# Performance work log

Hardware: AMD Instinct MI355X
Metric: run time of the kernel (lower is better)

The kernel has to match this reference:

```python
import jax, jax.numpy as jnp
import numpy as np

N_NODES = 200000
N_EDGES = 400000
N_GRAPHS = 4096
IN_DIM, HID_DIM, OUT_DIM, EDGE_DIM = 128, 256, 256, 16


def setup_inputs() -> dict:
    key = jax.random.key(0)
    ks = jax.random.split(key, 16)
    x = jax.random.normal(ks[0], (N_NODES, IN_DIM), dtype=jnp.float32)
    edge_attr = jax.random.normal(ks[1], (N_EDGES, EDGE_DIM), dtype=jnp.float32)
    edge_index = jax.random.randint(ks[2], (2, N_EDGES), 0, N_NODES, dtype=jnp.int64)
    batch = jnp.sort(jax.random.randint(ks[3], (N_NODES,), 0, N_GRAPHS, dtype=jnp.int64))

    def lin(k, fan_in, fan_out):
        bound = 1.0 / np.sqrt(fan_in)
        kw, kb = jax.random.split(k)
        W = jax.random.uniform(kw, (fan_in, fan_out), minval=-bound, maxval=bound, dtype=jnp.float32)
        b = jax.random.uniform(kb, (fan_out,), minval=-bound, maxval=bound, dtype=jnp.float32)
        return W, b

    We1, be1 = lin(ks[4], EDGE_DIM, IN_DIM)    # GINEConv1 edge projection
    W1a, b1a = lin(ks[5], IN_DIM, HID_DIM)     # conv1 MLP layer 1
    W1b, b1b = lin(ks[6], HID_DIM, HID_DIM)    # conv1 MLP layer 2
    We2, be2 = lin(ks[7], EDGE_DIM, HID_DIM)   # GINEConv2 edge projection
    W2a, b2a = lin(ks[8], HID_DIM, HID_DIM)    # conv2 MLP layer 1
    W2b, b2b = lin(ks[9], HID_DIM, OUT_DIM)    # conv2 MLP layer 2
    return {"x": x, "edge_attr": edge_attr,
            "We1": We1, "be1": be1, "W1a": W1a, "b1a": b1a, "W1b": W1b, "b1b": b1b,
            "We2": We2, "be2": be2, "W2a": W2a, "b2a": b2a, "W2b": W2b, "b2b": b2b,
            "edge_index": edge_index, "batch": batch}


def _gine_conv(x, edge_attr, src, dst, We, be, Wa, ba, Wb, bb):
    # messages: relu(x_j + lin_edge(e)), scatter-add into destination nodes
    e_proj = edge_attr @ We + be                      # [E, D]
    msg = jax.nn.relu(x[src] + e_proj)                # [E, D]
    aggr = jax.ops.segment_sum(msg, dst, num_segments=x.shape[0])  # [N, D]
    h = x + aggr                                      # (1 + eps) * x_i + aggr, eps=0
    h = jax.nn.relu(h @ Wa + ba)
    return h @ Wb + bb


def reference(x, edge_attr, We1, be1, W1a, b1a, W1b, b1b,
              We2, be2, W2a, b2a, W2b, b2b, edge_index, batch):
    src, dst = edge_index[0], edge_index[1]
    h = jax.nn.relu(_gine_conv(x, edge_attr, src, dst, We1, be1, W1a, b1a, W1b, b1b))
    h = jax.nn.relu(_gine_conv(h, edge_attr, src, dst, We2, be2, W2a, b2a, W2b, b2b))
    # global mean pool over graphs
    sums = jax.ops.segment_sum(h, batch, num_segments=N_GRAPHS)            # [G, D]
    counts = jax.ops.segment_sum(jnp.ones((h.shape[0],), h.dtype), batch,
                                 num_segments=N_GRAPHS)                    # [G]
    return sums / jnp.maximum(counts, 1.0)[:, None]
```

## Files before the change

kernel.cpp:

```cpp
#include <hip/hip_runtime.h>
#include <hip/hip_bf16.h>

typedef float f32x4 __attribute__((ext_vector_type(4)));
typedef float f32x2 __attribute__((ext_vector_type(2)));
typedef unsigned short u16x2 __attribute__((ext_vector_type(2)));
typedef unsigned short u16x4 __attribute__((ext_vector_type(4)));
typedef unsigned short u16x8 __attribute__((ext_vector_type(8)));
typedef short s16x8 __attribute__((ext_vector_type(8)));

#define NN 200000
#define NE 400000
#define NG 4096
#define SCHUNK 1024
#define NSCAN ((NN + SCHUNK - 1) / SCHUNK)

template<int C> struct VecT;
template<> struct VecT<2> { using T = u16x2; };
template<> struct VecT<4> { using T = u16x4; };

__device__ __forceinline__ unsigned short f2bf(float f) {
    union { float f; unsigned int u; } v; v.f = f;
    unsigned int r = v.u + 0x7FFF + ((v.u >> 16) & 1);
    return (unsigned short)(r >> 16);
}
__device__ __forceinline__ float bf2f(unsigned short b) {
    union { unsigned int u; float f; } v; v.u = ((unsigned int)b) << 16;
    return v.f;
}

__global__ void detect_i64(const int* __restrict__ ei, int* __restrict__ flag) {
    unsigned long long m = __ballot(ei[threadIdx.x * 2 + 1] == 0);
    if (threadIdx.x == 0) *flag = (~m == 0ULL) ? 1 : 0;
}
__device__ __forceinline__ int load_idx(const int* p, long long i, int f64) {
    return f64 ? (int)((const long long*)p)[i] : p[i];
}

__global__ __launch_bounds__(256) void bat_conv(const int* __restrict__ bat,
                                                const int* __restrict__ flag,
                                                int* __restrict__ bat32) {
    int i = blockIdx.x * 256 + threadIdx.x;
    if (i < NN) bat32[i] = *flag ? (int)((const long long*)bat)[i] : bat[i];
}

__global__ void wt_conv(const float* __restrict__ W, unsigned short* __restrict__ Wt,
                        int K, int N) {
    int tid = blockIdx.x * 256 + threadIdx.x;
    if (tid >= K * N) return;
    int n = tid / K, k = tid - n * K;
    Wt[tid] = f2bf(W[(size_t)k * N + n]);
}

__global__ __launch_bounds__(256) void x2bf(const float* __restrict__ x,
                                            unsigned short* __restrict__ xh) {
    long long i = ((long long)blockIdx.x * 256 + threadIdx.x) * 4;
    if (i >= (long long)NN * 128) return;
    f32x4 v = *(const f32x4*)(x + i);
    u16x4 o; o.x = f2bf(v.x); o.y = f2bf(v.y); o.z = f2bf(v.z); o.w = f2bf(v.w);
    *(u16x4*)(xh + i) = o;
}

__global__ __launch_bounds__(256) void ea_perm(const float* __restrict__ ea,
                                               const int* __restrict__ eidx,
                                               const int* __restrict__ totE_p,
                                               float* __restrict__ eac) {
    int j = blockIdx.x * 256 + threadIdx.x;
    if (j >= *totE_p) return;
    int e = eidx[j];
    if ((unsigned)e >= NE) e = 0;
    const float* s = ea + (size_t)e * 16;
    float* d = eac + (size_t)j * 16;
#pragma unroll
    for (int k = 0; k < 4; ++k)
        *(f32x4*)(d + k * 4) = *(const f32x4*)(s + k * 4);
}

__global__ __launch_bounds__(256) void hist_dst(const int* __restrict__ ei,
                                                const int* __restrict__ flag,
                                                int* __restrict__ deg) {
    int e = blockIdx.x * 256 + threadIdx.x;
    if (e >= NE) return;
    int f64 = *flag;
    int s = load_idx(ei, e, f64);
    int d = load_idx(ei, (long long)NE + e, f64);
    if ((unsigned)s < NN && (unsigned)d < NN) atomicAdd(&deg[d], 1);
}

__global__ __launch_bounds__(256) void scan_bsum(const int* __restrict__ deg,
                                                 int* __restrict__ bsum) {
    __shared__ int red[256];
    int t = threadIdx.x, base = blockIdx.x * SCHUNK + t * 4;
    int s = 0;
#pragma unroll
    for (int c = 0; c < 4; ++c) { int i = base + c; if (i < NN) s += deg[i]; }
    red[t] = s; __syncthreads();
    for (int o = 128; o > 0; o >>= 1) { if (t < o) red[t] += red[t + o]; __syncthreads(); }
    if (t == 0) bsum[blockIdx.x] = red[0];
}

__global__ void scan_carry(int* __restrict__ bsum, int* __restrict__ rowptr_end) {
    if (threadIdx.x == 0) {
        int run = 0;
        for (int i = 0; i < NSCAN; ++i) { int v = bsum[i]; bsum[i] = run; run += v; }
        *rowptr_end = run;
    }
}

__global__ __launch_bounds__(256) void scan_final(const int* __restrict__ deg,
                                                  const int* __restrict__ bsum,
                                                  int* __restrict__ rowptr,
                                                  int* __restrict__ cursor) {
    __shared__ int lds[256];
    int t = threadIdx.x, base = blockIdx.x * SCHUNK + t * 4;
    int v[4], s = 0;
#pragma unroll
    for (int c = 0; c < 4; ++c) { int i = base + c; v[c] = (i < NN) ? deg[i] : 0; s += v[c]; }
    lds[t] = s; __syncthreads();
    for (int o = 1; o < 256; o <<= 1) {
        int x = 0;
        if (t >= o) x = lds[t - o];
        __syncthreads();
        if (t >= o) lds[t] += x;
        __syncthreads();
    }
    int run = lds[t] - s + bsum[blockIdx.x];
#pragma unroll
    for (int c = 0; c < 4; ++c) {
        int i = base + c;
        if (i < NN) { rowptr[i] = run; cursor[i] = run; }
        run += v[c];
    }
}

__global__ __launch_bounds__(256) void fill_csr(const int* __restrict__ ei,
                                                const int* __restrict__ flag,
                                                int* __restrict__ cursor,
                                                int* __restrict__ srcs,
                                                int* __restrict__ eidx) {
    int e = blockIdx.x * 256 + threadIdx.x;
    if (e >= NE) return;
    int f64 = *flag;
    int s = load_idx(ei, e, f64);
    int d = load_idx(ei, (long long)NE + e, f64);
    if ((unsigned)s >= NN || (unsigned)d >= NN) return;
    int pos = atomicAdd(&cursor[d], 1);
    if ((unsigned)pos < NE) { srcs[pos] = s; eidx[pos] = e; }
}

template<int C, int U>
__global__ __launch_bounds__(256)
void msg_build(const unsigned short* __restrict__ xh,
               const float* __restrict__ eac,
               const float* __restrict__ We, const float* __restrict__ be,
               const int* __restrict__ srcs, const int* __restrict__ totE_p,
               unsigned short* __restrict__ M) {
    using XV = typename VecT<C>::T;
    constexpr int D = 64 * C;
    constexpr int C2 = C / 2;
    const int wid  = (blockIdx.x * 256 + threadIdx.x) >> 6;
    const int lane = threadIdx.x & 63;
    const int totE = *totE_p;
    const int col = lane * C;

    f32x2 w2[16][C2], bb2[C2];
#pragma unroll
    for (int k = 0; k < 16; ++k)
#pragma unroll
        for (int c = 0; c < C2; ++c)
            w2[k][c] = *(const f32x2*)(We + k * D + col + 2 * c);
#pragma unroll
    for (int c = 0; c < C2; ++c) bb2[c] = *(const f32x2*)(be + col + 2 * c);

    const int j0 = wid * U;
    int sv[U];
    XV xv[U];
#pragma unroll
    for (int u = 0; u < U; ++u) {
        int j = j0 + u;
        sv[u] = (j < totE) ? srcs[j] : -1;
    }
#pragma unroll
    for (int u = 0; u < U; ++u) {
        if ((unsigned)sv[u] < NN)
            xv[u] = *(const XV*)(xh + (size_t)sv[u] * D + col);
        else
            xv[u] = (XV)0;
    }
#pragma unroll
    for (int u = 0; u < U; ++u) {
        int j = j0 + u;
        if (j >= totE) continue;
        const float* eap = eac + (size_t)j * 16;
        f32x4 e0 = *(const f32x4*)eap;
        f32x4 e1 = *(const f32x4*)(eap + 4);
        f32x4 e2 = *(const f32x4*)(eap + 8);
        f32x4 e3 = *(const f32x4*)(eap + 12);
        f32x2 m2[C2];
#pragma unroll
        for (int c = 0; c < C2; ++c) {
            f32x2 xx; xx.x = bf2f(xv[u][2 * c]); xx.y = bf2f(xv[u][2 * c + 1]);
            m2[c] = bb2[c] + xx;
        }
#pragma unroll
        for (int k = 0; k < 4; ++k) {
            f32x2 k0; k0.x = e0[k]; k0.y = e0[k];
            f32x2 k1; k1.x = e1[k]; k1.y = e1[k];
            f32x2 k2; k2.x = e2[k]; k2.y = e2[k];
            f32x2 k3; k3.x = e3[k]; k3.y = e3[k];
#pragma unroll
            for (int c = 0; c < C2; ++c) {
                m2[c] += k0 * w2[k][c];
                m2[c] += k1 * w2[4 + k][c];
                m2[c] += k2 * w2[8 + k][c];
                m2[c] += k3 * w2[12 + k][c];
            }
        }
        XV o;
#pragma unroll
        for (int c = 0; c < C2; ++c) {
            o[2 * c]     = f2bf(fmaxf(m2[c].x, 0.f));
            o[2 * c + 1] = f2bf(fmaxf(m2[c].y, 0.f));
        }
        *(XV*)(M + (size_t)j * D + col) = o;
    }
}

template<int C>
__global__ __launch_bounds__(256)
void seg_sum(const unsigned short* __restrict__ M, const int* __restrict__ rowptr,
             const unsigned short* __restrict__ self, unsigned short* __restrict__ outp) {
    using XV = typename VecT<C>::T;
    constexpr int D = 64 * C;
    const int node = (blockIdx.x * 256 + threadIdx.x) >> 6;
    const int lane = threadIdx.x & 63;
    if (node >= NN) return;
    const int col = lane * C;
    int lo = rowptr[node], hi = rowptr[node + 1];
    if (lo > hi || (unsigned)hi > NE) { lo = 0; hi = 0; }

    float a[C];
    XV sv = *(const XV*)(self + (size_t)node * D + col);
#pragma unroll
    for (int c = 0; c < C; ++c) a[c] = bf2f(sv[c]);

    int j = lo;
    for (; j + 1 < hi; j += 2) {
        XV m0 = *(const XV*)(M + (size_t)j * D + col);
        XV m1 = *(const XV*)(M + (size_t)(j + 1) * D + col);
#pragma unroll
        for (int c = 0; c < C; ++c) a[c] += bf2f(m0[c]) + bf2f(m1[c]);
    }
    if (j < hi) {
        XV m0 = *(const XV*)(M + (size_t)j * D + col);
#pragma unroll
        for (int c = 0; c < C; ++c) a[c] += bf2f(m0[c]);
    }
    XV o;
#pragma unroll
    for (int c = 0; c < C; ++c) o[c] = f2bf(a[c]);
    *(XV*)(outp + (size_t)node * D + col) = o;
}

template<int K1, int MODE>
__global__ __launch_bounds__(256)
void gemm2_fused(const unsigned short* __restrict__ A,
                 const unsigned short* __restrict__ Wta, const float* __restrict__ ba,
                 const unsigned short* __restrict__ Wtb, const float* __restrict__ bb,
                 unsigned short* __restrict__ C,
                 float* __restrict__ sums, const int* __restrict__ bat32) {
    constexpr int LDT = 36;
    constexpr int LDM = 260;
    __shared__ unsigned short Us[64 * LDM];
    __shared__ unsigned short Bs[256 * LDT];
    const int m0 = blockIdx.x * 64;
    const int tid = threadIdx.x;
    const int wave = tid >> 6;
    const int lane = tid & 63;
    const int lm = lane & 15;
    const int lq = lane >> 4;
    const int nw = wave * 64;

    const int arow = tid >> 2;
    const int aseg = (tid & 3) * 8;
    const int brow = tid >> 1;
    const int bcol = (tid & 1) * 16;

    f32x4 acc[4][4] = {};

    for (int k0 = 0; k0 < K1; k0 += 32) {
        *(u16x8*)(Us + arow * LDT + aseg) =
            *(const u16x8*)(A + (size_t)(m0 + arow) * K1 + k0 + aseg);
        {
            const unsigned short* s0 = Wta + (size_t)brow * K1 + k0 + bcol;
            const unsigned short* s1 = Wta + (size_t)(brow + 128) * K1 + k0 + bcol;
            unsigned short* d0 = Bs + brow * LDT + bcol;
            unsigned short* d1 = Bs + (brow + 128) * LDT + bcol;
            *(u16x8*)(d0)     = *(const u16x8*)(s0);
            *(u16x8*)(d0 + 8) = *(const u16x8*)(s0 + 8);
            *(u16x8*)(d1)     = *(const u16x8*)(s1);
            *(u16x8*)(d1 + 8) = *(const u16x8*)(s1 + 8);
        }
        __syncthreads();
        s16x8 af[4], bf[4];
#pragma unroll
        for (int mt = 0; mt < 4; ++mt)
            af[mt] = *(const s16x8*)(Us + (mt * 16 + lm) * LDT + lq * 8);
#pragma unroll
        for (int nt = 0; nt < 4; ++nt)
            bf[nt] = *(const s16x8*)(Bs + (nw + nt * 16 + lm) * LDT + lq * 8);
#pragma unroll
        for (int mt = 0; mt < 4; ++mt)
#pragma unroll
            for (int nt = 0; nt < 4; ++nt)
                acc[mt][nt] = __builtin_amdgcn_mfma_f32_16x16x32_bf16(
                    af[mt], bf[nt], acc[mt][nt], 0, 0, 0);
        __syncthreads();
    }

#pragma unroll
    for (int mt = 0; mt < 4; ++mt) {
        const int row = mt * 16 + lq * 4;
#pragma unroll
        for (int nt = 0; nt < 4; ++nt) {
            int coln = nw + nt * 16 + lm;
            float bv = ba[coln];
#pragma unroll
            for (int r = 0; r < 4; ++r) {
                float v = fmaxf(acc[mt][nt][r] + bv, 0.f);
                Us[(row + r) * LDM + coln] = f2bf(v);
                acc[mt][nt][r] = 0.f;
            }
        }
    }
    __syncthreads();

    for (int k0 = 0; k0 < 256; k0 += 32) {
        {
            const unsigned short* s0 = Wtb + (size_t)brow * 256 + k0 + bcol;
            const unsigned short* s1 = Wtb + (size_t)(brow + 128) * 256 + k0 + bcol;
            unsigned short* d0 = Bs + brow * LDT + bcol;
            unsigned short* d1 = Bs + (brow + 128) * LDT + bcol;
            *(u16x8*)(d0)     = *(const u16x8*)(s0);
            *(u16x8*)(d0 + 8) = *(const u16x8*)(s0 + 8);
            *(u16x8*)(d1)     = *(const u16x8*)(s1);
            *(u16x8*)(d1 + 8) = *(const u16x8*)(s1 + 8);
        }
        __syncthreads();
        s16x8 af[4], bf[4];
#pragma unroll
        for (int mt = 0; mt < 4; ++mt)
            af[mt] = *(const s16x8*)(Us + (mt * 16 + lm) * LDM + k0 + lq * 8);
#pragma unroll
        for (int nt = 0; nt < 4; ++nt)
            bf[nt] = *(const s16x8*)(Bs + (nw + nt * 16 + lm) * LDT + lq * 8);
#pragma unroll
        for (int mt = 0; mt < 4; ++mt)
#pragma unroll
            for (int nt = 0; nt < 4; ++nt)
                acc[mt][nt] = __builtin_amdgcn_mfma_f32_16x16x32_bf16(
                    af[mt], bf[nt], acc[mt][nt], 0, 0, 0);
        __syncthreads();
    }

    if constexpr (MODE == 0) {
#pragma unroll
        for (int mt = 0; mt < 4; ++mt) {
            const int row = m0 + mt * 16 + lq * 4;
#pragma unroll
            for (int nt = 0; nt < 4; ++nt) {
                int coln = nw + nt * 16 + lm;
                float bv = bb[coln];
#pragma unroll
                for (int r = 0; r < 4; ++r) {
                    float v = fmaxf(acc[mt][nt][r] + bv, 0.f);
                    C[(size_t)(row + r) * 256 + coln] = f2bf(v);
                }
            }
        }
    } else {
        int g16[16];
#pragma unroll
        for (int mt = 0; mt < 4; ++mt)
#pragma unroll
            for (int r = 0; r < 4; ++r)
                g16[mt * 4 + r] = bat32[m0 + mt * 16 + lq * 4 + r];
#pragma unroll
        for (int nt = 0; nt < 4; ++nt) {
            int coln = nw + nt * 16 + lm;
            float bv = bb[coln];
            int curg = g16[0];
            float s = 0.f;
#pragma unroll
            for (int i = 0; i < 16; ++i) {
                float v = fmaxf(acc[i >> 2][nt][i & 3] + bv, 0.f);
                if (g16[i] != curg) {
                    if ((unsigned)curg < NG) atomicAdd(&sums[(size_t)curg * 256 + coln], s);
                    curg = g16[i]; s = 0.f;
                }
                s += v;
            }
            if ((unsigned)curg < NG) atomicAdd(&sums[(size_t)curg * 256 + coln], s);
        }
    }
}

__global__ __launch_bounds__(256)
void pool_div(const float* __restrict__ sums, const int* __restrict__ bat32,
              float* __restrict__ out) {
    int g = blockIdx.x;
    int a = 0, b = NN;
    while (a < b) { int m = (a + b) >> 1; if (bat32[m] < g) a = m + 1; else b = m; }
    int lo = a;
    b = NN;
    while (a < b) { int m = (a + b) >> 1; if (bat32[m] < g + 1) a = m + 1; else b = m; }
    float inv = 1.f / fmaxf((float)(a - lo), 1.f);
    out[(size_t)g * 256 + threadIdx.x] = sums[(size_t)g * 256 + threadIdx.x] * inv;
}

extern "C" void kernel_launch(void* const* d_in, const int* in_sizes, int n_in,
                              void* d_out, int out_size, void* d_ws, size_t ws_size,
                              hipStream_t stream) {
    const float* x   = (const float*)d_in[0];
    const float* ea  = (const float*)d_in[1];
    const float* We1 = (const float*)d_in[2];
    const float* be1 = (const float*)d_in[3];
    const float* W1a = (const float*)d_in[4];
    const float* b1a = (const float*)d_in[5];
    const float* W1b = (const float*)d_in[6];
    const float* b1b = (const float*)d_in[7];
    const float* We2 = (const float*)d_in[8];
    const float* be2 = (const float*)d_in[9];
    const float* W2a = (const float*)d_in[10];
    const float* b2a = (const float*)d_in[11];
    const float* W2b = (const float*)d_in[12];
    const float* b2b = (const float*)d_in[13];
    const int*   ei  = (const int*)d_in[14];
    const int*   bat = (const int*)d_in[15];
    float* out = (float*)d_out;

    char* ws = (char*)d_ws;
    const size_t SZH = (size_t)NN * 256 * 2;
    unsigned short* A  = (unsigned short*)ws;
    unsigned short* B  = (unsigned short*)(ws + SZH);
    char* Dr = ws + 3 * SZH;
    char* q = Dr;
    int* deg    = (int*)q; q += (size_t)NN * 4;
    int* rowptr = (int*)q; q += (size_t)(NN + 1) * 4;
    int* cursor = (int*)q; q += (size_t)NN * 4;
    int* srcs   = (int*)q; q += (size_t)NE * 4;
    int* eidx   = (int*)q; q += (size_t)NE * 4;
    int* bsum   = (int*)q; q += (size_t)NSCAN * 4;
    q = Dr + ((q - Dr + 63) & ~63ll);
    float*          eac = (float*)q; q += (size_t)NE * 16 * 4;
    unsigned short* xh  = (unsigned short*)q; q += (size_t)NN * 128 * 2;
    int*   bat32 = (int*)q;   q += (size_t)NN * 4;
    float* sums  = (float*)q; q += (size_t)NG * 256 * 4;
    char* p = ws + 4 * SZH;
    unsigned short* Wt1a = (unsigned short*)p; p += 128 * 256 * 2;
    unsigned short* Wt1b = (unsigned short*)p; p += 256 * 256 * 2;
    unsigned short* Wt2a = (unsigned short*)p; p += 256 * 256 * 2;
    unsigned short* Wt2b = (unsigned short*)p; p += 256 * 256 * 2;
    int* flag = (int*)p;

    detect_i64<<<1, 64, 0, stream>>>(ei, flag);
    bat_conv<<<(NN + 255) / 256, 256, 0, stream>>>(bat, flag, bat32);
    wt_conv<<<(128 * 256 + 255) / 256, 256, 0, stream>>>(W1a, Wt1a, 128, 256);
    wt_conv<<<(256 * 256 + 255) / 256, 256, 0, stream>>>(W1b, Wt1b, 256, 256);
    wt_conv<<<(256 * 256 + 255) / 256, 256, 0, stream>>>(W2a, Wt2a, 256, 256);
    wt_conv<<<(256 * 256 + 255) / 256, 256, 0, stream>>>(W2b, Wt2b, 256, 256);

    hipMemsetAsync(deg, 0, (size_t)NN * 4, stream);
    hipMemsetAsync(sums, 0, (size_t)NG * 256 * 4, stream);
    hist_dst<<<(NE + 255) / 256, 256, 0, stream>>>(ei, flag, deg);
    scan_bsum<<<NSCAN, 256, 0, stream>>>(deg, bsum);
    scan_carry<<<1, 64, 0, stream>>>(bsum, rowptr + NN);
    scan_final<<<NSCAN, 256, 0, stream>>>(deg, bsum, rowptr, cursor);
    fill_csr<<<(NE + 255) / 256, 256, 0, stream>>>(ei, flag, cursor, srcs, eidx);
    ea_perm<<<(NE + 255) / 256, 256, 0, stream>>>(ea, eidx, rowptr + NN, eac);
    x2bf<<<(NN * 128 / 4 + 255) / 256, 256, 0, stream>>>(x, xh);

    const int GM_BLK = NE / 32;
    const int GS_BLK = NN / 4;
    const int GG_BLK = NN / 64;

    msg_build<2, 8><<<GM_BLK, 256, 0, stream>>>(xh, eac, We1, be1, srcs, rowptr + NN, A);
    seg_sum<2><<<GS_BLK, 256, 0, stream>>>(A, rowptr, xh, B);
    gemm2_fused<128, 0><<<GG_BLK, 256, 0, stream>>>(B, Wt1a, b1a, Wt1b, b1b, A,
                                                    nullptr, nullptr);

    msg_build<4, 8><<<GM_BLK, 256, 0, stream>>>(A, eac, We2, be2, srcs, rowptr + NN, B);
    seg_sum<4><<<GS_BLK, 256, 0, stream>>>(B, rowptr, A, A);
    gemm2_fused<256, 1><<<GG_BLK, 256, 0, stream>>>(A, Wt2a, b2a, Wt2b, b2b, nullptr,
                                                    sums, bat32);

    pool_div<<<NG, 256, 0, stream>>>(sums, bat32, out);
}
```

Measured before the change: 913.7 us.

## Load GEMM weights directly to registers with prefetch, drop LDS B staging

The fused two-layer GEMM kernel stops staging weight tiles through shared memory. Each wave now loads its B fragments straight from global memory into registers, prefetching the next k-slice (including the first slice of the second weight matrix) while the current MFMAs run. The whole A tile is loaded into LDS once up front, which removes the per-iteration syncthreads, and launch bounds now request 3 blocks per CU. The cost is redundant global/L2 weight reads per block and more register pressure from the double-buffered fragments.

```diff
diff --git a/kernel.cpp b/kernel.cpp
--- a/kernel.cpp
+++ b/kernel.cpp
@@ -262,16 +262,15 @@
 }
 
 template<int K1, int MODE>
-__global__ __launch_bounds__(256)
+__global__ __launch_bounds__(256, 3)
 void gemm2_fused(const unsigned short* __restrict__ A,
                  const unsigned short* __restrict__ Wta, const float* __restrict__ ba,
                  const unsigned short* __restrict__ Wtb, const float* __restrict__ bb,
                  unsigned short* __restrict__ C,
                  float* __restrict__ sums, const int* __restrict__ bat32) {
-    constexpr int LDT = 36;
+    constexpr int LDA = K1 + 4;
     constexpr int LDM = 260;
     __shared__ unsigned short Us[64 * LDM];
-    __shared__ unsigned short Bs[256 * LDT];
     const int m0 = blockIdx.x * 64;
     const int tid = threadIdx.x;
     const int wave = tid >> 6;
@@ -280,42 +279,46 @@
     const int lq = lane >> 4;
     const int nw = wave * 64;
 
-    const int arow = tid >> 2;
-    const int aseg = (tid & 3) * 8;
-    const int brow = tid >> 1;
-    const int bcol = (tid & 1) * 16;
+    {
+        const int arow = tid >> 2;
+        const int acol = (tid & 3) * 8;
+        const unsigned short* src = A + (size_t)(m0 + arow) * K1;
+        unsigned short* dst = Us + arow * LDA;
+#pragma unroll
+        for (int c = 0; c < K1 / 32; ++c)
+            *(u16x8*)(dst + acol + c * 32) = *(const u16x8*)(src + acol + c * 32);
+    }
+
+    auto ldb = [&](const unsigned short* W, int KW, int k0, s16x8* bf) {
+#pragma unroll
+        for (int nt = 0; nt < 4; ++nt)
+            bf[nt] = *(const s16x8*)(W + (size_t)(nw + nt * 16 + lm) * KW + k0 + lq * 8);
+    };
 
     f32x4 acc[4][4] = {};
+    s16x8 bcur[4], bnxt[4];
+
+    ldb(Wta, K1, 0, bcur);
+    __syncthreads();
 
     for (int k0 = 0; k0 < K1; k0 += 32) {
-        *(u16x8*)(Us + arow * LDT + aseg) =
-            *(const u16x8*)(A + (size_t)(m0 + arow) * K1 + k0 + aseg);
-        {
-            const unsigned short* s0 = Wta + (size_t)brow * K1 + k0 + bcol;
-            const unsigned short* s1 = Wta + (size_t)(brow + 128) * K1 + k0 + bcol;
-            unsigned short* d0 = Bs + brow * LDT + bcol;
-            unsigned short* d1 = Bs + (brow + 128) * LDT + bcol;
-            *(u16x8*)(d0)     = *(const u16x8*)(s0);
-            *(u16x8*)(d0 + 8) = *(const u16x8*)(s0 + 8);
-            *(u16x8*)(d1)     = *(const u16x8*)(s1);
-            *(u16x8*)(d1 + 8) = *(const u16x8*)(s1 + 8);
-        }
-        __syncthreads();
-        s16x8 af[4], bf[4];
+        if (k0 + 32 < K1) ldb(Wta, K1, k0 + 32, bnxt);
+        else              ldb(Wtb, 256, 0, bnxt);
+        s16x8 af[4];
 #pragma unroll
         for (int mt = 0; mt < 4; ++mt)
-            af[mt] = *(const s16x8*)(Us + (mt * 16 + lm) * LDT + lq * 8);
-#pragma unroll
-        for (int nt = 0; nt < 4; ++nt)
-            bf[nt] = *(const s16x8*)(Bs + (nw + nt * 16 + lm) * LDT + lq * 8);
+            af[mt] = *(const s16x8*)(Us + (mt * 16 + lm) * LDA + k0 + lq * 8);
 #pragma unroll
         for (int mt = 0; mt < 4; ++mt)
 #pragma unroll
             for (int nt = 0; nt < 4; ++nt)
                 acc[mt][nt] = __builtin_amdgcn_mfma_f32_16x16x32_bf16(
-                    af[mt], bf[nt], acc[mt][nt], 0, 0, 0);
-        __syncthreads();
-    }
+                    af[mt], bcur[nt], acc[mt][nt], 0, 0, 0);
+#pragma unroll
+        for (int nt = 0; nt < 4; ++nt) bcur[nt] = bnxt[nt];
+    }
+
+    __syncthreads();
 
 #pragma unroll
     for (int mt = 0; mt < 4; ++mt) {
@@ -335,31 +338,19 @@
     __syncthreads();
 
     for (int k0 = 0; k0 < 256; k0 += 32) {
-        {
-            const unsigned short* s0 = Wtb + (size_t)brow * 256 + k0 + bcol;
-            const unsigned short* s1 = Wtb + (size_t)(brow + 128) * 256 + k0 + bcol;
-            unsigned short* d0 = Bs + brow * LDT + bcol;
-            unsigned short* d1 = Bs + (brow + 128) * LDT + bcol;
-            *(u16x8*)(d0)     = *(const u16x8*)(s0);
-            *(u16x8*)(d0 + 8) = *(const u16x8*)(s0 + 8);
-            *(u16x8*)(d1)     = *(const u16x8*)(s1);
-            *(u16x8*)(d1 + 8) = *(const u16x8*)(s1 + 8);
-        }
-        __syncthreads();
-        s16x8 af[4], bf[4];
+        if (k0 + 32 < 256) ldb(Wtb, 256, k0 + 32, bnxt);
+        s16x8 af[4];
 #pragma unroll
         for (int mt = 0; mt < 4; ++mt)
             af[mt] = *(const s16x8*)(Us + (mt * 16 + lm) * LDM + k0 + lq * 8);
 #pragma unroll
-        for (int nt = 0; nt < 4; ++nt)
-            bf[nt] = *(const s16x8*)(Bs + (nw + nt * 16 + lm) * LDT + lq * 8);
-#pragma unroll
         for (int mt = 0; mt < 4; ++mt)
 #pragma unroll
             for (int nt = 0; nt < 4; ++nt)
                 acc[mt][nt] = __builtin_amdgcn_mfma_f32_16x16x32_bf16(
-                    af[mt], bf[nt], acc[mt][nt], 0, 0, 0);
-        __syncthreads();
+                    af[mt], bcur[nt], acc[mt][nt], 0, 0, 0);
+#pragma unroll
+        for (int nt = 0; nt < 4; ++nt) bcur[nt] = bnxt[nt];
     }
 
     if constexpr (MODE == 0) {
```

Result: faster. 866.3 us (-5.2%).
